# Optimization experiments

Hardware: AMD Instinct MI355X
Metric: run time of the kernel (lower is better)

## Reference

```python
import jax, jax.numpy as jnp
import numpy as np

H = 1024      # hidden_size
NH = 16       # num_heads
HD = H // NH  # head_dim
FF = 4 * H    # ffn hidden


def setup_inputs() -> dict:
    key = jax.random.key(0)
    ks = jax.random.split(key, 11)
    s = 1.0 / np.sqrt(H)
    inp = {
        "x": jax.random.normal(ks[0], (2, 2048, H), dtype=jnp.float32),
        "Wq": jax.random.uniform(ks[1], (H, H), jnp.float32, -s, s),
        "Wk": jax.random.uniform(ks[2], (H, H), jnp.float32, -s, s),
        "Wv": jax.random.uniform(ks[3], (H, H), jnp.float32, -s, s),
        "Wo": jax.random.uniform(ks[4], (H, H), jnp.float32, -s, s),
        "ln1_g": jnp.ones((H,), jnp.float32),
        "ln1_b": jnp.zeros((H,), jnp.float32),
        "ln2_g": jnp.ones((H,), jnp.float32),
        "ln2_b": jnp.zeros((H,), jnp.float32),
        "W1": jax.random.uniform(ks[5], (H, FF), jnp.float32, -s, s),
        "b1": jnp.zeros((FF,), jnp.float32),
        "W2": jax.random.uniform(ks[6], (FF, H), jnp.float32, -1.0 / np.sqrt(FF), 1.0 / np.sqrt(FF)),
        "b2": jnp.zeros((H,), jnp.float32),
    }
    return inp


def _layernorm(x, g, b, eps=1e-5):
    mu = jnp.mean(x, axis=-1, keepdims=True)
    var = jnp.mean(jnp.square(x - mu), axis=-1, keepdims=True)
    return (x - mu) * jax.lax.rsqrt(var + eps) * g + b


def reference(x, Wq, Wk, Wv, Wo, ln1_g, ln1_b, ln2_g, ln2_b, W1, b1, W2, b2):
    bsz, seq, _ = x.shape
    h = _layernorm(x, ln1_g, ln1_b)
    # project and split heads: [b, s, H] -> [b, nh, s, hd]
    def split(t):
        return t.reshape(bsz, seq, NH, HD).transpose(0, 2, 1, 3)
    q = split(h @ Wq.T)
    k = split(h @ Wk.T)
    v = split(h @ Wv.T)
    scores = jnp.einsum("bhqd,bhkd->bhqk", q, k) / jnp.sqrt(jnp.float32(HD))
    probs = jax.nn.softmax(scores, axis=-1)
    attn = jnp.einsum("bhqk,bhkd->bhqd", probs, v)
    attn = attn.transpose(0, 2, 1, 3).reshape(bsz, seq, H)
    x = x + attn @ Wo.T
    h2 = _layernorm(x, ln2_g, ln2_b)
    ffn = jax.nn.gelu(h2 @ W1 + b1, approximate=False) @ W2 + b2
    return x + ffn
```

## Files before the change

kernel.cpp:

```cpp
#include <hip/hip_runtime.h>
#include <stdint.h>
#include <math.h>

typedef float f32x4 __attribute__((ext_vector_type(4)));
typedef __bf16 bf16x8 __attribute__((ext_vector_type(8)));

#define DEVI __device__ __forceinline__

#if __has_builtin(__builtin_amdgcn_exp2f)
#define EXP2(x) __builtin_amdgcn_exp2f(x)
#else
#define EXP2(x) exp2f(x)
#endif

#define LOG2E 1.44269504f

DEVI unsigned short f2bf(float f) {
  union { float f; unsigned int u; } c; c.f = f;
  unsigned int u = c.u;
  return (unsigned short)((u + 0x7FFFu + ((u >> 16) & 1u)) >> 16);
}

DEVI unsigned short f2bf_fast(float f) {
  union { float f; unsigned int u; } c; c.f = f;
  return (unsigned short)((c.u + 0x8000u) >> 16);
}

DEVI void gll16(const void* g, void* l) {
  __builtin_amdgcn_global_load_lds(
      (const __attribute__((address_space(1))) void*)g,
      (__attribute__((address_space(3))) void*)l,
      16, 0, 0);
}

__global__ __launch_bounds__(256) void f32_to_bf16_k(
    const float* __restrict__ in, unsigned short* __restrict__ out, int n4) {
  int i = blockIdx.x * 256 + threadIdx.x;
  if (i >= n4) return;
  float4 v = ((const float4*)in)[i];
  ushort4 ov;
  ov.x = f2bf(v.x); ov.y = f2bf(v.y); ov.z = f2bf(v.z); ov.w = f2bf(v.w);
  ((ushort4*)out)[i] = ov;
}

__global__ __launch_bounds__(256) void transpose_f32_bf16(
    const float* __restrict__ in, unsigned short* __restrict__ out, int R, int C) {
  __shared__ float tile[32][33];
  int bc = blockIdx.x * 32, br = blockIdx.y * 32;
  int tx = threadIdx.x & 31, ty = threadIdx.x >> 5;
#pragma unroll
  for (int i = 0; i < 32; i += 8)
    tile[ty + i][tx] = in[(size_t)(br + ty + i) * C + bc + tx];
  __syncthreads();
#pragma unroll
  for (int i = 0; i < 32; i += 8)
    out[(size_t)(bc + ty + i) * R + br + tx] = f2bf(tile[tx][ty + i]);
}

__global__ __launch_bounds__(256) void vtrans(
    const unsigned short* __restrict__ QKV, unsigned short* __restrict__ Vt) {
  int stile = blockIdx.x;
  int bh = blockIdx.y;
  int b = bh >> 4, h = bh & 15;
  __shared__ unsigned short tile[64][68];
  const unsigned short* src =
      QKV + ((size_t)(b * 2048 + stile * 64)) * 3072 + 2048 + h * 64;
  int t = threadIdx.x;
#pragma unroll
  for (int i = 0; i < 16; i++) {
    int e = i * 256 + t; int s = e >> 6, d = e & 63;
    tile[s][d] = src[(size_t)s * 3072 + d];
  }
  __syncthreads();
  unsigned short* dst = Vt + (size_t)bh * 64 * 2048 + stile * 64;
#pragma unroll
  for (int i = 0; i < 16; i++) {
    int e = i * 256 + t; int d = e >> 6, s = e & 63;
    dst[(size_t)d * 2048 + s] = tile[s][d];
  }
}

__global__ __launch_bounds__(256) void layernorm_bf16(
    const float* __restrict__ x, const float* __restrict__ g,
    const float* __restrict__ be, unsigned short* __restrict__ out) {
  const int row = blockIdx.x;
  const int t = threadIdx.x;
  const float4 v = ((const float4*)(x + (size_t)row * 1024))[t];
  float s = v.x + v.y + v.z + v.w;
  float s2 = v.x * v.x + v.y * v.y + v.z * v.z + v.w * v.w;
#pragma unroll
  for (int d = 32; d > 0; d >>= 1) {
    s += __shfl_down(s, d);
    s2 += __shfl_down(s2, d);
  }
  __shared__ float ps[4], ps2[4], st[2];
  const int lane = t & 63, wave = t >> 6;
  if (lane == 0) { ps[wave] = s; ps2[wave] = s2; }
  __syncthreads();
  if (t == 0) {
    float S = ps[0] + ps[1] + ps[2] + ps[3];
    float S2 = ps2[0] + ps2[1] + ps2[2] + ps2[3];
    float mu = S * (1.0f / 1024.0f);
    float var = S2 * (1.0f / 1024.0f) - mu * mu;
    st[0] = mu; st[1] = rsqrtf(var + 1e-5f);
  }
  __syncthreads();
  float mu = st[0], inv = st[1];
  float4 gv = ((const float4*)g)[t];
  float4 bv = ((const float4*)be)[t];
  ushort4 ov;
  ov.x = f2bf((v.x - mu) * inv * gv.x + bv.x);
  ov.y = f2bf((v.y - mu) * inv * gv.y + bv.y);
  ov.z = f2bf((v.z - mu) * inv * gv.z + bv.z);
  ov.w = f2bf((v.w - mu) * inv * gv.w + bv.w);
  ((ushort4*)(out + (size_t)row * 1024))[t] = ov;
}

DEVI float gelu_f(float x) {
  float a = x * (2.3022082f + 0.1029432f * x * x);
  return x / (1.0f + EXP2(-a));
}

template <int EPI, int TM, int TN>
__global__ __launch_bounds__(256, (TM >= 256 ? 2 : 4)) void gemm_bt(
    const unsigned short* __restrict__ A, const unsigned short* __restrict__ B,
    int M, int N, int K, float* __restrict__ outF, unsigned short* __restrict__ outB,
    const float* __restrict__ res, const float* __restrict__ bias) {
  __shared__ __align__(16) unsigned short As[2][TM * 32];
  __shared__ __align__(16) unsigned short Bs[2][TN * 32];
  constexpr int MF = TM / 32;
  constexpr int NF = TN / 32;
  const int t = threadIdx.x;
  const int lane = t & 63, wave = t >> 6;
  const int wr = wave >> 1, wc = wave & 1;
  const int l15 = lane & 15, lg = lane >> 4;
  const int sl = (t & 7) ^ ((t >> 3) & 7);
  const int srow2 = ((t >> 3) << 1) + (sl >> 2);
  const int scol2 = (sl & 3) * 8;
  const int gx = gridDim.x;
  const int nwg = gx * gridDim.y;
  const int orig = blockIdx.y * gx + blockIdx.x;
  const int swz = (orig & 7) * (nwg >> 3) + (orig >> 3);
  const int bx = swz % gx, by = swz / gx;
  const size_t aBase = (size_t)by * TM * K;
  const size_t bBase = (size_t)bx * TN * K;
  f32x4 acc[MF][NF] = {};

  auto stage = [&](int buf, int kt) {
#pragma unroll
    for (int i = 0; i < TM / 64; i++)
      gll16(A + aBase + (size_t)(srow2 + i * 64) * K + kt + scol2,
            (char*)&As[buf][0] + i * 4096 + t * 16);
#pragma unroll
    for (int i = 0; i < TN / 64; i++)
      gll16(B + bBase + (size_t)(srow2 + i * 64) * K + kt + scol2,
            (char*)&Bs[buf][0] + i * 4096 + t * 16);
  };

  stage(0, 0);
  __syncthreads();
  const int nk = K >> 5;
  for (int ki = 0; ki < nk; ki++) {
    const int cur = ki & 1;
    if (ki + 1 < nk) stage(cur ^ 1, (ki + 1) << 5);
    bf16x8 af[MF], bfv[NF];
#pragma unroll
    for (int m = 0; m < MF; m++) {
      const int R = wr * (TM / 2) + m * 16 + l15;
      const int r = R >> 1;
      const int ps = (((R & 1) << 2) | lg) ^ (r & 7);
      af[m] = *(const bf16x8*)&As[cur][r * 64 + ps * 8];
    }
#pragma unroll
    for (int n = 0; n < NF; n++) {
      const int R = wc * (TN / 2) + n * 16 + l15;
      const int r = R >> 1;
      const int ps = (((R & 1) << 2) | lg) ^ (r & 7);
      bfv[n] = *(const bf16x8*)&Bs[cur][r * 64 + ps * 8];
    }
#pragma unroll
    for (int m = 0; m < MF; m++)
#pragma unroll
      for (int n = 0; n < NF; n++)
        acc[m][n] = __builtin_amdgcn_mfma_f32_16x16x32_bf16(af[m], bfv[n], acc[m][n], 0, 0, 0);
    __syncthreads();
  }
  const int rowB = by * TM + wr * (TM / 2);
  const int colB = bx * TN + wc * (TN / 2);
#pragma unroll
  for (int m = 0; m < MF; m++) {
#pragma unroll
    for (int n = 0; n < NF; n++) {
#pragma unroll
      for (int r = 0; r < 4; r++) {
        int gm = rowB + m * 16 + lg * 4 + r;
        int gn = colB + n * 16 + l15;
        float c = acc[m][n][r];
        size_t idx = (size_t)gm * N + gn;
        if (EPI == 0) {
          outB[idx] = f2bf(c);
        } else if (EPI == 1) {
          outF[idx] = res[idx] + c;
        } else if (EPI == 2) {
          outB[idx] = f2bf(gelu_f(c + bias[gn]));
        } else {
          outF[idx] = res[idx] + c + bias[gn];
        }
      }
    }
  }
}

__global__ __launch_bounds__(256) void attn_flash(
    const unsigned short* __restrict__ QKV, const unsigned short* __restrict__ Vt,
    unsigned short* __restrict__ attnO) {
  __shared__ __align__(16) unsigned short Ks[2][64 * 64];
  __shared__ __align__(16) unsigned short Vs[2][64 * 64];
  __shared__ __align__(16) unsigned short Ps[128 * 64];
  const int t = threadIdx.x;
  const int lane = t & 63, wave = t >> 6;
  const int l15 = lane & 15, lg = lane >> 4;
  const int bid = blockIdx.x;
  const int swzb = (bid & 7) * 64 + (bid >> 3);
  const int qt = swzb & 15;
  const int bh = swzb >> 4;
  const int b = bh >> 4, h = bh & 15;
  const size_t qkvBase = (size_t)b * 2048 * 3072 + (size_t)h * 64;

  bf16x8 aq[2][2];
#pragma unroll
  for (int fi = 0; fi < 2; fi++) {
    int qrow = qt * 128 + wave * 32 + fi * 16 + l15;
    const unsigned short* qp = QKV + qkvBase + (size_t)qrow * 3072;
#pragma unroll
    for (int kc = 0; kc < 2; kc++) {
      aq[fi][kc] = *(const bf16x8*)(qp + kc * 32 + lg * 8);
#pragma unroll
      for (int j = 0; j < 8; j++)
        aq[fi][kc][j] = (__bf16)((float)aq[fi][kc][j] * 0.125f);
    }
  }
  bf16x8 onesf;
#pragma unroll
  for (int j = 0; j < 8; j++) onesf[j] = (__bf16)1.0f;

  const unsigned short* Kg = QKV + qkvBase + 1024;
  const unsigned short* Vg = Vt + (size_t)bh * 64 * 2048;

  f32x4 o[2][4] = {};
  f32x4 ol[2] = {};
  const float M2 = 4.0f * LOG2E;

  const int srow = t >> 3;
  const int scb = (t & 7) * 16;
  const int e = (scb ^ ((srow & 7) << 4)) >> 1;

  auto stage = [&](int buf, int kt) {
    gll16(Kg + (size_t)(kt * 64 + srow) * 3072 + e, (char*)&Ks[buf][0] + t * 16);
    gll16(Kg + (size_t)(kt * 64 + srow + 32) * 3072 + e, (char*)&Ks[buf][0] + 4096 + t * 16);
    gll16(Vg + (size_t)srow * 2048 + kt * 64 + e, (char*)&Vs[buf][0] + t * 16);
    gll16(Vg + (size_t)(srow + 32) * 2048 + kt * 64 + e, (char*)&Vs[buf][0] + 4096 + t * 16);
  };

  stage(0, 0);
  __syncthreads();

  for (int kt = 0; kt < 32; kt++) {
    const int cur = kt & 1;
    if (kt < 31) stage(cur ^ 1, kt + 1);

    f32x4 s[2][4] = {};
#pragma unroll
    for (int n = 0; n < 4; n++) {
#pragma unroll
      for (int kc = 0; kc < 2; kc++) {
        int r = n * 16 + l15;
        int cb = (kc * 64 + lg * 16) ^ ((r & 7) << 4);
        bf16x8 bk = *(const bf16x8*)&Ks[cur][r * 64 + (cb >> 1)];
        s[0][n] = __builtin_amdgcn_mfma_f32_16x16x32_bf16(aq[0][kc], bk, s[0][n], 0, 0, 0);
        s[1][n] = __builtin_amdgcn_mfma_f32_16x16x32_bf16(aq[1][kc], bk, s[1][n], 0, 0, 0);
      }
    }

#pragma unroll
    for (int fi = 0; fi < 2; fi++) {
      const int q0 = wave * 32 + fi * 16 + lg * 4;
#pragma unroll
      for (int n = 0; n < 4; n++)
#pragma unroll
        for (int r = 0; r < 4; r++) {
          int q = q0 + r;
          int cb = ((n * 16 + l15) * 2) ^ ((q & 7) << 4);
          float p = EXP2(__builtin_fmaf(s[fi][n][r], LOG2E, -M2));
          Ps[q * 64 + (cb >> 1)] = f2bf_fast(p);
        }
    }

#pragma unroll
    for (int kc = 0; kc < 2; kc++) {
      bf16x8 pa[2];
#pragma unroll
      for (int fi = 0; fi < 2; fi++) {
        int qr = wave * 32 + fi * 16 + l15;
        int cbp = (kc * 64 + lg * 16) ^ ((qr & 7) << 4);
        pa[fi] = *(const bf16x8*)&Ps[qr * 64 + (cbp >> 1)];
        ol[fi] = __builtin_amdgcn_mfma_f32_16x16x32_bf16(pa[fi], onesf, ol[fi], 0, 0, 0);
      }
#pragma unroll
      for (int n = 0; n < 4; n++) {
        int dr = n * 16 + l15;
        int cbv = (kc * 64 + lg * 16) ^ ((dr & 7) << 4);
        bf16x8 bv = *(const bf16x8*)&Vs[cur][dr * 64 + (cbv >> 1)];
        o[0][n] = __builtin_amdgcn_mfma_f32_16x16x32_bf16(pa[0], bv, o[0][n], 0, 0, 0);
        o[1][n] = __builtin_amdgcn_mfma_f32_16x16x32_bf16(pa[1], bv, o[1][n], 0, 0, 0);
      }
    }
    __syncthreads();
  }

#pragma unroll
  for (int fi = 0; fi < 2; fi++) {
    const int qrow0 = qt * 128 + wave * 32 + fi * 16;
    unsigned short* op = attnO + ((size_t)(b * 2048 + qrow0)) * 1024 + h * 64;
    float inv[4];
#pragma unroll
    for (int r = 0; r < 4; r++) inv[r] = 1.0f / ol[fi][r];
#pragma unroll
    for (int n = 0; n < 4; n++)
#pragma unroll
      for (int r = 0; r < 4; r++) {
        int q = lg * 4 + r;
        op[(size_t)q * 1024 + n * 16 + l15] = f2bf(o[fi][n][r] * inv[r]);
      }
  }
}

extern "C" void kernel_launch(void* const* d_in, const int* in_sizes, int n_in,
                              void* d_out, int out_size, void* d_ws, size_t ws_size,
                              hipStream_t stream) {
  const float* x = (const float*)d_in[0];
  const float* Wq = (const float*)d_in[1];
  const float* Wk = (const float*)d_in[2];
  const float* Wv = (const float*)d_in[3];
  const float* Wo = (const float*)d_in[4];
  const float* ln1g = (const float*)d_in[5];
  const float* ln1b = (const float*)d_in[6];
  const float* ln2g = (const float*)d_in[7];
  const float* ln2b = (const float*)d_in[8];
  const float* W1 = (const float*)d_in[9];
  const float* b1 = (const float*)d_in[10];
  const float* W2 = (const float*)d_in[11];
  const float* b2 = (const float*)d_in[12];
  float* out = (float*)d_out;

  char* ws = (char*)d_ws;
  size_t off = 0;
  auto alloc = [&](size_t bytes) {
    void* p = ws + off;
    off += (bytes + 255) & ~(size_t)255;
    return p;
  };
  unsigned short* WB = (unsigned short*)alloc(3072ull * 1024 * 2);
  unsigned short* WoB = (unsigned short*)alloc(1024ull * 1024 * 2);
  unsigned short* W1t = (unsigned short*)alloc(4096ull * 1024 * 2);
  unsigned short* W2t = (unsigned short*)alloc(1024ull * 4096 * 2);
  unsigned short* hb = (unsigned short*)alloc(4096ull * 1024 * 2);
  unsigned short* QKV = (unsigned short*)alloc(4096ull * 3072 * 2);
  unsigned short* attnb = (unsigned short*)alloc(4096ull * 1024 * 2);
  unsigned short* Vtb = (unsigned short*)alloc(32ull * 64 * 2048 * 2);
  float* x2 = (float*)alloc(4096ull * 1024 * 4);
  unsigned short* ffnb = QKV;
  unsigned short* h2b = hb;

  f32_to_bf16_k<<<1024, 256, 0, stream>>>(Wq, WB, 262144);
  f32_to_bf16_k<<<1024, 256, 0, stream>>>(Wk, WB + 1048576, 262144);
  f32_to_bf16_k<<<1024, 256, 0, stream>>>(Wv, WB + 2097152, 262144);
  f32_to_bf16_k<<<1024, 256, 0, stream>>>(Wo, WoB, 262144);
  transpose_f32_bf16<<<dim3(128, 32), 256, 0, stream>>>(W1, W1t, 1024, 4096);
  transpose_f32_bf16<<<dim3(32, 128), 256, 0, stream>>>(W2, W2t, 4096, 1024);
  layernorm_bf16<<<4096, 256, 0, stream>>>(x, ln1g, ln1b, hb);
  gemm_bt<0, 256, 128><<<dim3(24, 16), 256, 0, stream>>>(hb, WB, 4096, 3072, 1024,
                                                         nullptr, QKV, nullptr, nullptr);
  vtrans<<<dim3(32, 32), 256, 0, stream>>>(QKV, Vtb);
  attn_flash<<<512, 256, 0, stream>>>(QKV, Vtb, attnb);
  gemm_bt<1, 64, 128><<<dim3(8, 64), 256, 0, stream>>>(attnb, WoB, 4096, 1024, 1024,
                                                       x2, nullptr, x, nullptr);
  layernorm_bf16<<<4096, 256, 0, stream>>>(x2, ln2g, ln2b, h2b);
  gemm_bt<2, 256, 128><<<dim3(32, 16), 256, 0, stream>>>(h2b, W1t, 4096, 4096, 1024,
                                                         nullptr, ffnb, nullptr, b1);
  gemm_bt<3, 64, 128><<<dim3(8, 64), 256, 0, stream>>>(ffnb, W2t, 4096, 1024, 4096,
                                                       out, nullptr, x2, b2);
}
```

Baseline: 251.5 us.

## Add 256x256 tile, 512-thread GEMM with BK=64 for QKV and FFN1 projections

Adds a new GEMM kernel that uses 256x256 output tiles, 8 waves, and a K-step of 64. Its global-to-LDS loads are split into four parts and interleaved with the MFMA phases, and it raises wave priority around the MFMA blocks. The QKV and W1 projections move to this kernel to get more operand reuse per LDS load and fewer workgroups. The trade-off is a much larger LDS footprint (128 KB per block), so occupancy drops and tail effects grow with the small grids (192 and 256 blocks). The older GEMM is reduced to the fp32 residual epilogues.

```diff
diff --git a/kernel.cpp b/kernel.cpp
--- a/kernel.cpp
+++ b/kernel.cpp
@@ -121,10 +121,110 @@
   return x / (1.0f + EXP2(-a));
 }
 
+template <int EPI>
+__global__ __launch_bounds__(512, 2) void gemm256(
+    const unsigned short* __restrict__ A, const unsigned short* __restrict__ B,
+    int M, int N, int K, unsigned short* __restrict__ outB,
+    const float* __restrict__ bias) {
+  __shared__ __align__(16) unsigned short As[2][256 * 64];
+  __shared__ __align__(16) unsigned short Bs[2][256 * 64];
+  const int t = threadIdx.x;
+  const int lane = t & 63, wave = t >> 6;
+  const int wm = wave >> 2, wn = wave & 3;
+  const int l15 = lane & 15, lg = lane >> 4;
+  const int e = 8 * ((t & 7) ^ ((t >> 3) & 7));
+  const int srow = t >> 3;
+  const int gx = gridDim.x;
+  const int nwg = gx * gridDim.y;
+  const int orig = blockIdx.y * gx + blockIdx.x;
+  const int swz = (orig & 7) * (nwg >> 3) + (orig >> 3);
+  const int bx = swz % gx, by = swz / gx;
+  const size_t aBase = (size_t)by * 256 * K;
+  const size_t bBase = (size_t)bx * 256 * K;
+
+  f32x4 acc[8][4] = {};
+
+  auto stagePart = [&](int buf, int kcol, int j) {
+    gll16(A + aBase + (size_t)(j * 64 + srow) * K + kcol + e,
+          (char*)&As[buf][0] + j * 8192 + t * 16);
+    gll16(B + bBase + (size_t)(j * 64 + srow) * K + kcol + e,
+          (char*)&Bs[buf][0] + j * 8192 + t * 16);
+  };
+
+  const int nk = K >> 6;
+#pragma unroll
+  for (int j = 0; j < 4; j++) stagePart(0, 0, j);
+
+  for (int kt = 0; kt < nk; kt++) {
+    const int cur = kt & 1;
+    const bool more = (kt + 1 < nk);
+    asm volatile("s_barrier" ::: "memory");
+    if (more) {
+      stagePart(cur ^ 1, (kt + 1) << 6, 0);
+      asm volatile("s_waitcnt vmcnt(2)" ::: "memory");
+    } else {
+      asm volatile("s_waitcnt vmcnt(0)" ::: "memory");
+    }
+    asm volatile("s_barrier" ::: "memory");
+#pragma unroll
+    for (int ph = 0; ph < 4; ph++) {
+      const int mh = ph >> 1, nh = ph & 1;
+      if (more && ph < 3) stagePart(cur ^ 1, (kt + 1) << 6, ph + 1);
+      bf16x8 af[4][2], bfv[2][2];
+#pragma unroll
+      for (int mi = 0; mi < 4; mi++) {
+        const int R = wm * 128 + mh * 64 + mi * 16 + l15;
+#pragma unroll
+        for (int ks = 0; ks < 2; ks++) {
+          const int pc = (ks * 64 + lg * 16) ^ ((R & 7) << 4);
+          af[mi][ks] = *(const bf16x8*)((const char*)&As[cur][0] + R * 128 + pc);
+        }
+      }
+#pragma unroll
+      for (int ni = 0; ni < 2; ni++) {
+        const int R = wn * 64 + nh * 32 + ni * 16 + l15;
+#pragma unroll
+        for (int ks = 0; ks < 2; ks++) {
+          const int pc = (ks * 64 + lg * 16) ^ ((R & 7) << 4);
+          bfv[ni][ks] = *(const bf16x8*)((const char*)&Bs[cur][0] + R * 128 + pc);
+        }
+      }
+      __builtin_amdgcn_s_setprio(1);
+#pragma unroll
+      for (int mi = 0; mi < 4; mi++)
+#pragma unroll
+        for (int ni = 0; ni < 2; ni++)
+#pragma unroll
+          for (int ks = 0; ks < 2; ks++)
+            acc[mh * 4 + mi][nh * 2 + ni] = __builtin_amdgcn_mfma_f32_16x16x32_bf16(
+                af[mi][ks], bfv[ni][ks], acc[mh * 4 + mi][nh * 2 + ni], 0, 0, 0);
+      __builtin_amdgcn_s_setprio(0);
+    }
+  }
+
+  const int rowB = by * 256 + wm * 128;
+  const int colB = bx * 256 + wn * 64;
+#pragma unroll
+  for (int m = 0; m < 8; m++) {
+#pragma unroll
+    for (int n = 0; n < 4; n++) {
+      const int gn = colB + n * 16 + l15;
+      float bb = (EPI == 2) ? bias[gn] : 0.0f;
+#pragma unroll
+      for (int r = 0; r < 4; r++) {
+        const int gm = rowB + m * 16 + lg * 4 + r;
+        const size_t idx = (size_t)gm * N + gn;
+        if (EPI == 0) outB[idx] = f2bf(acc[m][n][r]);
+        else          outB[idx] = f2bf(gelu_f(acc[m][n][r] + bb));
+      }
+    }
+  }
+}
+
 template <int EPI, int TM, int TN>
-__global__ __launch_bounds__(256, (TM >= 256 ? 2 : 4)) void gemm_bt(
+__global__ __launch_bounds__(256, 4) void gemm_bt(
     const unsigned short* __restrict__ A, const unsigned short* __restrict__ B,
-    int M, int N, int K, float* __restrict__ outF, unsigned short* __restrict__ outB,
+    int M, int N, int K, float* __restrict__ outF,
     const float* __restrict__ res, const float* __restrict__ bias) {
   __shared__ __align__(16) unsigned short As[2][TM * 32];
   __shared__ __align__(16) unsigned short Bs[2][TN * 32];
@@ -197,15 +297,8 @@
         int gn = colB + n * 16 + l15;
         float c = acc[m][n][r];
         size_t idx = (size_t)gm * N + gn;
-        if (EPI == 0) {
-          outB[idx] = f2bf(c);
-        } else if (EPI == 1) {
-          outF[idx] = res[idx] + c;
-        } else if (EPI == 2) {
-          outB[idx] = f2bf(gelu_f(c + bias[gn]));
-        } else {
-          outF[idx] = res[idx] + c + bias[gn];
-        }
+        if (EPI == 1) outF[idx] = res[idx] + c;
+        else          outF[idx] = res[idx] + c + bias[gn];
       }
     }
   }
@@ -379,15 +472,15 @@
   transpose_f32_bf16<<<dim3(128, 32), 256, 0, stream>>>(W1, W1t, 1024, 4096);
   transpose_f32_bf16<<<dim3(32, 128), 256, 0, stream>>>(W2, W2t, 4096, 1024);
   layernorm_bf16<<<4096, 256, 0, stream>>>(x, ln1g, ln1b, hb);
-  gemm_bt<0, 256, 128><<<dim3(24, 16), 256, 0, stream>>>(hb, WB, 4096, 3072, 1024,
-                                                         nullptr, QKV, nullptr, nullptr);
+  gemm256<0><<<dim3(12, 16), 512, 0, stream>>>(hb, WB, 4096, 3072, 1024,
+                                               QKV, nullptr);
   vtrans<<<dim3(32, 32), 256, 0, stream>>>(QKV, Vtb);
   attn_flash<<<512, 256, 0, stream>>>(QKV, Vtb, attnb);
   gemm_bt<1, 64, 128><<<dim3(8, 64), 256, 0, stream>>>(attnb, WoB, 4096, 1024, 1024,
-                                                       x2, nullptr, x, nullptr);
+                                                       x2, x, nullptr);
   layernorm_bf16<<<4096, 256, 0, stream>>>(x2, ln2g, ln2b, h2b);
-  gemm_bt<2, 256, 128><<<dim3(32, 16), 256, 0, stream>>>(h2b, W1t, 4096, 4096, 1024,
-                                                         nullptr, ffnb, nullptr, b1);
+  gemm256<2><<<dim3(16, 16), 512, 0, stream>>>(h2b, W1t, 4096, 4096, 1024,
+                                               ffnb, b1);
   gemm_bt<3, 64, 128><<<dim3(8, 64), 256, 0, stream>>>(ffnb, W2t, 4096, 1024, 4096,
-                                                       out, nullptr, x2, b2);
-}
+                                                       out, x2, b2);
+}
```

Measured after the change: 269.9 us. 1.07x slower.
